# Optimization experiments

Measured on AMD Instinct MI355X. Metric: run time of the kernel, lower is better.

Reference implementation:

```python
import jax, jax.numpy as jnp
import numpy as np

B, L, C = 32, 4096, 64
PL, PC = 64, 16          # patch sizes along L and C
NP = 256                 # num_patches
OUT = 512                # output_dim
FS = 1000.0              # sampling frequency -> T = 1/FS


def setup_inputs() -> dict:
    key = jax.random.key(0)
    ks = jax.random.split(key, 7)
    d_in = PL * (PC * 2)
    return {
        "x": jax.random.normal(ks[0], (B, L, C), dtype=jnp.float32),
        "start_L": jax.random.randint(ks[1], (B, NP), 0, L - PL + 1, dtype=jnp.int32),
        "start_C": jax.random.randint(ks[2], (B, NP), 0, C - PC + 1, dtype=jnp.int32),
        "w1": jax.random.normal(ks[3], (OUT, d_in), dtype=jnp.float32) / np.sqrt(d_in),
        "b1": jax.random.normal(ks[4], (OUT,), dtype=jnp.float32) * 0.01,
        "w2": jax.random.normal(ks[5], (OUT, OUT), dtype=jnp.float32) / np.sqrt(OUT),
        "b2": jax.random.normal(ks[6], (OUT,), dtype=jnp.float32) * 0.01,
    }


def reference(x, start_L, start_C, w1, b1, w2, b2):
    T = 1.0 / FS
    t = jnp.arange(L, dtype=jnp.float32) * T                      # [L]

    # patch index grids (wrapping, as in the torch module)
    idx_L = (start_L[:, :, None] + jnp.arange(PL, dtype=jnp.int32)) % L   # [B,NP,PL]
    idx_C = (start_C[:, :, None] + jnp.arange(PC, dtype=jnp.int32)) % C   # [B,NP,PC]

    # double gather: patches[b,p,i,j] = x[b, idx_L[b,p,i], idx_C[b,p,j]]
    b_idx = jnp.arange(B, dtype=jnp.int32)[:, None, None, None]
    patches = x[b_idx, idx_L[:, :, :, None], idx_C[:, :, None, :]]        # [B,NP,PL,PC]

    # time embedding gathered with the same L indices, broadcast over PC
    t_patches = jnp.broadcast_to(t[idx_L][:, :, :, None], (B, NP, PL, PC))

    feats = jnp.concatenate([patches, t_patches], axis=-1)                # [B,NP,PL,2*PC]
    feats = feats.reshape(B, NP, PL * 2 * PC)

    h = jnp.einsum('bpd,od->bpo', feats, w1) + b1
    h = jax.nn.silu(h)
    out = jnp.einsum('bpo,qo->bpq', h, w2) + b2                           # [B,NP,OUT]
    return out
```

## Files before the change

### kernel.cpp

```cpp
#include <hip/hip_runtime.h>
#include <hip/hip_bf16.h>
#include <stdint.h>

#define LL   4096
#define CCH  64
#define DOUT 512
#define MM   8192
#define TT   0.001f

using bf16 = __hip_bfloat16;
typedef __attribute__((ext_vector_type(8))) short bf16x8;
typedef __attribute__((ext_vector_type(4))) float f32x4;

__device__ __forceinline__ uint2 pack4_bf16(float a, float b, float c, float d) {
    union { bf16 h[4]; uint2 u; } p;
    p.h[0] = __float2bfloat16(a);
    p.h[1] = __float2bfloat16(b);
    p.h[2] = __float2bfloat16(c);
    p.h[3] = __float2bfloat16(d);
    return p.u;
}

__device__ __forceinline__ void dma16(const bf16* g, bf16* l) {
    __builtin_amdgcn_global_load_lds(
        (const __attribute__((address_space(1))) void*)g,
        (__attribute__((address_space(3))) void*)l, 16, 0, 0);
}


__global__ __launch_bounds__(256) void prep(
    const float* __restrict__ w1, const float* __restrict__ b1,
    const float* __restrict__ w2,
    bf16* __restrict__ w1gs, bf16* __restrict__ w2gs,
    float* __restrict__ A1, float* __restrict__ C1)
{
    const int blk = blockIdx.x;
    if (blk < 512) {
        int g     = blk * 256 + threadIdx.x;
        int col_g = g >> 8;
        int k     = (g & 255) * 4;
        int l     = k >> 4, j = k & 15;
        float4 v = *(const float4*)(w1 + (size_t)col_g * 2048 + l * 32 + j);
        int kc = k >> 6, nt = col_g >> 7, colL = col_g & 127, u = (k >> 3) & 7;
        size_t idx = (size_t)(kc * 4 + nt) * 8192 + colL * 64
                   + ((u ^ (colL & 7)) * 8) + (k & 7);
        *(uint2*)(w1gs + idx) = pack4_bf16(v.x, v.y, v.z, v.w);
    } else if (blk < 768) {
        int g     = (blk - 512) * 256 + threadIdx.x;
        int col_g = g >> 7;
        int k     = (g & 127) * 4;
        float4 v = *(const float4*)(w2 + (size_t)col_g * 512 + k);
        int kc = k >> 6, nt = col_g >> 7, colL = col_g & 127, u = (k >> 3) & 7;
        size_t idx = (size_t)(kc * 4 + nt) * 8192 + colL * 64
                   + ((u ^ (colL & 7)) * 8) + (k & 7);
        *(uint2*)(w2gs + idx) = pack4_bf16(v.x, v.y, v.z, v.w);
    } else {
        const int o = (blk - 768) * 4 + (threadIdx.x >> 6);
        const int l = threadIdx.x & 63;
        const float* wr = w1 + (size_t)o * 2048 + l * 32 + 16;
        float s0 = 0.f;
#pragma unroll
        for (int j = 0; j < 16; ++j) s0 += wr[j];
        float s1 = (float)l * s0;
#pragma unroll
        for (int off = 32; off > 0; off >>= 1) {
            s0 += __shfl_down(s0, off);
            s1 += __shfl_down(s1, off);
        }
        if (l == 0) {
            A1[o] = TT * s0;
            C1[o] = b1[o] + TT * s1;
        }
    }
}

__global__ __launch_bounds__(256) void gather(
    const float* __restrict__ x, const int* __restrict__ sLg,
    const int* __restrict__ sCg, bf16* __restrict__ Ag)
{
    const int tg = blockIdx.x * 256 + threadIdx.x;
    const int r  = tg >> 6;
    const int l  = tg & 63;
    const int b  = r >> 8;
    const int sl = sLg[r], sc = sCg[r];
    const float* src = x + ((size_t)b * LL + sl + l) * CCH + sc;
    float4 v0 = *(const float4*)(src);
    float4 v1 = *(const float4*)(src + 4);
    float4 v2 = *(const float4*)(src + 8);
    float4 v3 = *(const float4*)(src + 12);
    bf16* dst = Ag + (size_t)(l >> 2) * 524288 + (size_t)r * 64;
    const int u0 = (l & 3) * 2;
    const int p0 = u0 ^ (r & 7), p1 = (u0 + 1) ^ (r & 7);
    *(uint2*)(dst + p0 * 8)     = pack4_bf16(v0.x, v0.y, v0.z, v0.w);
    *(uint2*)(dst + p0 * 8 + 4) = pack4_bf16(v1.x, v1.y, v1.z, v1.w);
    *(uint2*)(dst + p1 * 8)     = pack4_bf16(v2.x, v2.y, v2.z, v2.w);
    *(uint2*)(dst + p1 * 8 + 4) = pack4_bf16(v3.x, v3.y, v3.z, v3.w);
}

template<int NIT>
__device__ __forceinline__ void gemm_kloop(
    const bf16* aSrc, const bf16* bSrc, size_t aChunkStride,
    bf16 (&As)[2][8192], bf16 (&Bs)[2][8192],
    int wave, int fr, int fq, int wr, int wc, f32x4 acc[4][2])
{
    auto STAGE = [&](int buf, int kc) {
        const bf16* as = aSrc + (size_t)kc * aChunkStride;
        const bf16* bs = bSrc + (size_t)kc * 32768;
        dma16(as,       &As[buf][wave * 1024]);
        dma16(as + 512, &As[buf][wave * 1024 + 512]);
        dma16(bs,       &Bs[buf][wave * 1024]);
        dma16(bs + 512, &Bs[buf][wave * 1024 + 512]);
    };
    STAGE(0, 0);
    STAGE(1, 1);
#pragma unroll
    for (int it = 0; it < NIT; ++it) {
        if (it < NIT - 1) { asm volatile("s_waitcnt vmcnt(4)" ::: "memory"); }
        else              { asm volatile("s_waitcnt vmcnt(0)" ::: "memory"); }
        __builtin_amdgcn_sched_barrier(0);
        __builtin_amdgcn_s_barrier();
        __builtin_amdgcn_sched_barrier(0);
        const bf16* ab = &As[it & 1][0];
        const bf16* bb = &Bs[it & 1][0];
#pragma unroll
        for (int kk = 0; kk < 2; ++kk) {
            const int u = kk * 4 + fq;
            bf16x8 af[4], bf[2];
#pragma unroll
            for (int i = 0; i < 4; ++i) {
                const int row = wr * 64 + i * 16 + fr;
                af[i] = *(const bf16x8*)&ab[row * 64 + ((u ^ (row & 7)) * 8)];
            }
#pragma unroll
            for (int j = 0; j < 2; ++j) {
                const int col = wc * 32 + j * 16 + fr;
                bf[j] = *(const bf16x8*)&bb[col * 64 + ((u ^ (col & 7)) * 8)];
            }
#pragma unroll
            for (int i = 0; i < 4; ++i)
#pragma unroll
                for (int j = 0; j < 2; ++j)
                    acc[i][j] = __builtin_amdgcn_mfma_f32_16x16x32_bf16(
                        af[i], bf[j], acc[i][j], 0, 0, 0);
        }
        __builtin_amdgcn_sched_barrier(0);
        asm volatile("s_waitcnt lgkmcnt(0)" ::: "memory");
        __builtin_amdgcn_s_barrier();
        __builtin_amdgcn_sched_barrier(0);
        if (it < NIT - 2) STAGE(it & 1, it + 2);
    }
}

__global__ __launch_bounds__(512, 2) void gemm1(
    const bf16* __restrict__ Ag, const bf16* __restrict__ w1gs,
    const int* __restrict__ sLg, const float* __restrict__ A1,
    const float* __restrict__ C1, bf16* __restrict__ Hg)
{
    __shared__ __align__(16) bf16 As[2][8192];
    __shared__ __align__(16) bf16 Bs[2][8192];
    const int t = threadIdx.x, lane = t & 63, wave = t >> 6;
    const int fr = lane & 15, fq = lane >> 4;
    const int wr = wave >> 2, wc = wave & 3;
    const int nt = blockIdx.x & 3, mt = blockIdx.x >> 2;

    float avv[2], cvv[2];
#pragma unroll
    for (int j = 0; j < 2; ++j) {
        const int colG = nt * 128 + wc * 32 + j * 16 + fr;
        avv[j] = A1[colG];
        cvv[j] = C1[colG];
    }
    float slr[4][4];
#pragma unroll
    for (int i = 0; i < 4; ++i)
#pragma unroll
        for (int rr = 0; rr < 4; ++rr)
            slr[i][rr] = (float)sLg[mt * 128 + wr * 64 + i * 16 + fq * 4 + rr];

    const bf16* aSrc = Ag   + (size_t)mt * 8192 + wave * 1024 + lane * 8;
    const bf16* bSrc = w1gs + (size_t)nt * 8192 + wave * 1024 + lane * 8;
    f32x4 acc[4][2] = {};
    gemm_kloop<16>(aSrc, bSrc, 524288, As, Bs, wave, fr, fq, wr, wc, acc);

#pragma unroll
    for (int i = 0; i < 4; ++i)
#pragma unroll
        for (int j = 0; j < 2; ++j) {
            const int colG = nt * 128 + wc * 32 + j * 16 + fr;
            const int kc2  = colG >> 6;
            const int kcol = colG & 63;
            const int u    = kcol >> 3;
#pragma unroll
            for (int rr = 0; rr < 4; ++rr) {
                const int rG = mt * 128 + wr * 64 + i * 16 + fq * 4 + rr;
                float v = acc[i][j][rr] + slr[i][rr] * avv[j] + cvv[j];
                v = v / (1.0f + __expf(-v));
                Hg[(size_t)kc2 * 524288 + (size_t)rG * 64
                   + ((u ^ (rG & 7)) * 8) + (kcol & 7)] = __float2bfloat16(v);
            }
        }
}

__global__ __launch_bounds__(512, 2) void gemm2(
    const bf16* __restrict__ Hg, const bf16* __restrict__ w2gs,
    const float* __restrict__ b2, float* __restrict__ out)
{
    __shared__ __align__(16) bf16 As[2][8192];
    __shared__ __align__(16) bf16 Bs[2][8192];
    const int t = threadIdx.x, lane = t & 63, wave = t >> 6;
    const int fr = lane & 15, fq = lane >> 4;
    const int wr = wave >> 2, wc = wave & 3;
    const int nt = blockIdx.x & 3, mt = blockIdx.x >> 2;

    float bvv[2];
#pragma unroll
    for (int j = 0; j < 2; ++j)
        bvv[j] = b2[nt * 128 + wc * 32 + j * 16 + fr];

    const bf16* aSrc = Hg   + (size_t)mt * 8192 + wave * 1024 + lane * 8;
    const bf16* bSrc = w2gs + (size_t)nt * 8192 + wave * 1024 + lane * 8;
    f32x4 acc[4][2] = {};
    gemm_kloop<8>(aSrc, bSrc, 524288, As, Bs, wave, fr, fq, wr, wc, acc);

#pragma unroll
    for (int i = 0; i < 4; ++i)
#pragma unroll
        for (int j = 0; j < 2; ++j) {
            const int colG = nt * 128 + wc * 32 + j * 16 + fr;
#pragma unroll
            for (int rr = 0; rr < 4; ++rr) {
                const int rG = mt * 128 + wr * 64 + i * 16 + fq * 4 + rr;
                out[(size_t)rG * 512 + colG] = acc[i][j][rr] + bvv[j];
            }
        }
}

extern "C" void kernel_launch(void* const* d_in, const int* in_sizes, int n_in,
                              void* d_out, int out_size, void* d_ws, size_t ws_size,
                              hipStream_t stream)
{
    const float* x  = (const float*)d_in[0];
    const int*   sL = (const int*)  d_in[1];
    const int*   sC = (const int*)  d_in[2];
    const float* w1 = (const float*)d_in[3];
    const float* b1 = (const float*)d_in[4];
    const float* w2 = (const float*)d_in[5];
    const float* b2 = (const float*)d_in[6];
    float* out = (float*)d_out;

    char* ws = (char*)d_ws;
    bf16*  w1gs = (bf16*)ws;
    bf16*  w2gs = (bf16*)(ws + (1 << 20));
    float* A1   = (float*)(ws + (1 << 20) + (1 << 19));
    float* C1   = A1 + DOUT;
    bf16*  Ag   = (bf16*)(ws + (2  << 20));
    bf16*  Hg   = (bf16*)(ws + (18 << 20));

    gather<<<2048, 256, 0, stream>>>(x, sL, sC, Ag);
    prep<<<896, 256, 0, stream>>>(w1, b1, w2, w1gs, w2gs, A1, C1);
    gemm1<<<256, 512, 0, stream>>>(Ag, w1gs, sL, A1, C1, Hg);
    gemm2<<<256, 512, 0, stream>>>(Hg, w2gs, b2, out);
}
```

Measured before the change: 131.9 us.

## Merge gather and prep kernels, triple-buffer GEMM K-loop, stagger K start per block

Fuses the gather and weight-prep kernels into one launch to drop a kernel boundary. The GEMM K-loop moves from double to triple buffering in LDS, with three stages in flight and matching vmcnt waits, to hide more global-to-LDS latency. Each block also starts its K traversal at a rotated chunk offset so concurrent blocks read different K chunks and spread memory traffic. LDS use per block grows by half (96KB at 2 blocks/CU), which may pressure occupancy.

```diff
diff --git a/kernel.cpp b/kernel.cpp
--- a/kernel.cpp
+++ b/kernel.cpp
@@ -28,15 +28,38 @@
 }
 
 
-__global__ __launch_bounds__(256) void prep(
+__global__ __launch_bounds__(256) void gprep(
+    const float* __restrict__ x, const int* __restrict__ sLg,
+    const int* __restrict__ sCg, bf16* __restrict__ Ag,
     const float* __restrict__ w1, const float* __restrict__ b1,
     const float* __restrict__ w2,
     bf16* __restrict__ w1gs, bf16* __restrict__ w2gs,
     float* __restrict__ A1, float* __restrict__ C1)
 {
     const int blk = blockIdx.x;
-    if (blk < 512) {
-        int g     = blk * 256 + threadIdx.x;
+    if (blk < 2048) {
+        const int tg = blk * 256 + threadIdx.x;
+        const int r  = tg >> 6;
+        const int l  = tg & 63;
+        const int b  = r >> 8;
+        const int sl = sLg[r], sc = sCg[r];
+        const float* src = x + ((size_t)b * LL + sl + l) * CCH + sc;
+        float4 v0 = *(const float4*)(src);
+        float4 v1 = *(const float4*)(src + 4);
+        float4 v2 = *(const float4*)(src + 8);
+        float4 v3 = *(const float4*)(src + 12);
+        bf16* dst = Ag + (size_t)(l >> 2) * 524288 + (size_t)r * 64;
+        const int u0 = (l & 3) * 2;
+        const int p0 = u0 ^ (r & 7), p1 = (u0 + 1) ^ (r & 7);
+        *(uint2*)(dst + p0 * 8)     = pack4_bf16(v0.x, v0.y, v0.z, v0.w);
+        *(uint2*)(dst + p0 * 8 + 4) = pack4_bf16(v1.x, v1.y, v1.z, v1.w);
+        *(uint2*)(dst + p1 * 8)     = pack4_bf16(v2.x, v2.y, v2.z, v2.w);
+        *(uint2*)(dst + p1 * 8 + 4) = pack4_bf16(v3.x, v3.y, v3.z, v3.w);
+        return;
+    }
+    const int pb = blk - 2048;
+    if (pb < 512) {
+        int g     = pb * 256 + threadIdx.x;
         int col_g = g >> 8;
         int k     = (g & 255) * 4;
         int l     = k >> 4, j = k & 15;
@@ -45,8 +68,8 @@
         size_t idx = (size_t)(kc * 4 + nt) * 8192 + colL * 64
                    + ((u ^ (colL & 7)) * 8) + (k & 7);
         *(uint2*)(w1gs + idx) = pack4_bf16(v.x, v.y, v.z, v.w);
-    } else if (blk < 768) {
-        int g     = (blk - 512) * 256 + threadIdx.x;
+    } else if (pb < 768) {
+        int g     = (pb - 512) * 256 + threadIdx.x;
         int col_g = g >> 7;
         int k     = (g & 127) * 4;
         float4 v = *(const float4*)(w2 + (size_t)col_g * 512 + k);
@@ -55,7 +78,7 @@
                    + ((u ^ (colL & 7)) * 8) + (k & 7);
         *(uint2*)(w2gs + idx) = pack4_bf16(v.x, v.y, v.z, v.w);
     } else {
-        const int o = (blk - 768) * 4 + (threadIdx.x >> 6);
+        const int o = (pb - 768) * 4 + (threadIdx.x >> 6);
         const int l = threadIdx.x & 63;
         const float* wr = w1 + (size_t)o * 2048 + l * 32 + 16;
         float s0 = 0.f;
@@ -74,37 +97,15 @@
     }
 }
 
-__global__ __launch_bounds__(256) void gather(
-    const float* __restrict__ x, const int* __restrict__ sLg,
-    const int* __restrict__ sCg, bf16* __restrict__ Ag)
-{
-    const int tg = blockIdx.x * 256 + threadIdx.x;
-    const int r  = tg >> 6;
-    const int l  = tg & 63;
-    const int b  = r >> 8;
-    const int sl = sLg[r], sc = sCg[r];
-    const float* src = x + ((size_t)b * LL + sl + l) * CCH + sc;
-    float4 v0 = *(const float4*)(src);
-    float4 v1 = *(const float4*)(src + 4);
-    float4 v2 = *(const float4*)(src + 8);
-    float4 v3 = *(const float4*)(src + 12);
-    bf16* dst = Ag + (size_t)(l >> 2) * 524288 + (size_t)r * 64;
-    const int u0 = (l & 3) * 2;
-    const int p0 = u0 ^ (r & 7), p1 = (u0 + 1) ^ (r & 7);
-    *(uint2*)(dst + p0 * 8)     = pack4_bf16(v0.x, v0.y, v0.z, v0.w);
-    *(uint2*)(dst + p0 * 8 + 4) = pack4_bf16(v1.x, v1.y, v1.z, v1.w);
-    *(uint2*)(dst + p1 * 8)     = pack4_bf16(v2.x, v2.y, v2.z, v2.w);
-    *(uint2*)(dst + p1 * 8 + 4) = pack4_bf16(v3.x, v3.y, v3.z, v3.w);
-}
-
 template<int NIT>
 __device__ __forceinline__ void gemm_kloop(
-    const bf16* aSrc, const bf16* bSrc, size_t aChunkStride,
-    bf16 (&As)[2][8192], bf16 (&Bs)[2][8192],
+    const bf16* aSrc, const bf16* bSrc, size_t aStride, int kc0,
+    bf16 (&As)[3][8192], bf16 (&Bs)[3][8192],
     int wave, int fr, int fq, int wr, int wc, f32x4 acc[4][2])
 {
-    auto STAGE = [&](int buf, int kc) {
-        const bf16* as = aSrc + (size_t)kc * aChunkStride;
+    auto STAGE = [&](int buf, int it) {
+        const int kc = (kc0 + it) & (NIT - 1);
+        const bf16* as = aSrc + (size_t)kc * aStride;
         const bf16* bs = bSrc + (size_t)kc * 32768;
         dma16(as,       &As[buf][wave * 1024]);
         dma16(as + 512, &As[buf][wave * 1024 + 512]);
@@ -113,15 +114,19 @@
     };
     STAGE(0, 0);
     STAGE(1, 1);
+    STAGE(2, 2);
 #pragma unroll
     for (int it = 0; it < NIT; ++it) {
-        if (it < NIT - 1) { asm volatile("s_waitcnt vmcnt(4)" ::: "memory"); }
-        else              { asm volatile("s_waitcnt vmcnt(0)" ::: "memory"); }
+        if (it < NIT - 2)       { asm volatile("s_waitcnt vmcnt(8)" ::: "memory"); }
+        else if (it == NIT - 2) { asm volatile("s_waitcnt vmcnt(4)" ::: "memory"); }
+        else                    { asm volatile("s_waitcnt vmcnt(0)" ::: "memory"); }
         __builtin_amdgcn_sched_barrier(0);
         __builtin_amdgcn_s_barrier();
         __builtin_amdgcn_sched_barrier(0);
-        const bf16* ab = &As[it & 1][0];
-        const bf16* bb = &Bs[it & 1][0];
+        const int kc = (kc0 + it) & (NIT - 1);
+        (void)kc;
+        const bf16* ab = &As[it % 3][0];
+        const bf16* bb = &Bs[it % 3][0];
 #pragma unroll
         for (int kk = 0; kk < 2; ++kk) {
             const int u = kk * 4 + fq;
@@ -147,7 +152,7 @@
         asm volatile("s_waitcnt lgkmcnt(0)" ::: "memory");
         __builtin_amdgcn_s_barrier();
         __builtin_amdgcn_sched_barrier(0);
-        if (it < NIT - 2) STAGE(it & 1, it + 2);
+        if (it < NIT - 3) STAGE(it % 3, it + 3);
     }
 }
 
@@ -156,12 +161,13 @@
     const int* __restrict__ sLg, const float* __restrict__ A1,
     const float* __restrict__ C1, bf16* __restrict__ Hg)
 {
-    __shared__ __align__(16) bf16 As[2][8192];
-    __shared__ __align__(16) bf16 Bs[2][8192];
+    __shared__ __align__(16) bf16 As[3][8192];
+    __shared__ __align__(16) bf16 Bs[3][8192];
     const int t = threadIdx.x, lane = t & 63, wave = t >> 6;
     const int fr = lane & 15, fq = lane >> 4;
     const int wr = wave >> 2, wc = wave & 3;
     const int nt = blockIdx.x & 3, mt = blockIdx.x >> 2;
+    const int kc0 = (blockIdx.x >> 3) & 15;
 
     float avv[2], cvv[2];
 #pragma unroll
@@ -180,7 +186,7 @@
     const bf16* aSrc = Ag   + (size_t)mt * 8192 + wave * 1024 + lane * 8;
     const bf16* bSrc = w1gs + (size_t)nt * 8192 + wave * 1024 + lane * 8;
     f32x4 acc[4][2] = {};
-    gemm_kloop<16>(aSrc, bSrc, 524288, As, Bs, wave, fr, fq, wr, wc, acc);
+    gemm_kloop<16>(aSrc, bSrc, 524288, kc0, As, Bs, wave, fr, fq, wr, wc, acc);
 
 #pragma unroll
     for (int i = 0; i < 4; ++i)
@@ -205,12 +211,13 @@
     const bf16* __restrict__ Hg, const bf16* __restrict__ w2gs,
     const float* __restrict__ b2, float* __restrict__ out)
 {
-    __shared__ __align__(16) bf16 As[2][8192];
-    __shared__ __align__(16) bf16 Bs[2][8192];
+    __shared__ __align__(16) bf16 As[3][8192];
+    __shared__ __align__(16) bf16 Bs[3][8192];
     const int t = threadIdx.x, lane = t & 63, wave = t >> 6;
     const int fr = lane & 15, fq = lane >> 4;
     const int wr = wave >> 2, wc = wave & 3;
     const int nt = blockIdx.x & 3, mt = blockIdx.x >> 2;
+    const int kc0 = (blockIdx.x >> 3) & 7;
 
     float bvv[2];
 #pragma unroll
@@ -220,7 +227,7 @@
     const bf16* aSrc = Hg   + (size_t)mt * 8192 + wave * 1024 + lane * 8;
     const bf16* bSrc = w2gs + (size_t)nt * 8192 + wave * 1024 + lane * 8;
     f32x4 acc[4][2] = {};
-    gemm_kloop<8>(aSrc, bSrc, 524288, As, Bs, wave, fr, fq, wr, wc, acc);
+    gemm_kloop<8>(aSrc, bSrc, 524288, kc0, As, Bs, wave, fr, fq, wr, wc, acc);
 
 #pragma unroll
     for (int i = 0; i < 4; ++i)
@@ -256,8 +263,8 @@
     bf16*  Ag   = (bf16*)(ws + (2  << 20));
     bf16*  Hg   = (bf16*)(ws + (18 << 20));
 
-    gather<<<2048, 256, 0, stream>>>(x, sL, sC, Ag);
-    prep<<<896, 256, 0, stream>>>(w1, b1, w2, w1gs, w2gs, A1, C1);
+    gprep<<<2944, 256, 0, stream>>>(x, sL, sC, Ag, w1, b1, w2,
+                                    w1gs, w2gs, A1, C1);
     gemm1<<<256, 512, 0, stream>>>(Ag, w1gs, sL, A1, C1, Hg);
     gemm2<<<256, 512, 0, stream>>>(Hg, w2gs, b2, out);
 }
```

New measurement: 129.8 us. About the same (-1.6%).
